# Optimization experiments

Hardware: AMD Instinct MI355X
Metric: run time of the kernel (lower is better)

The kernel has to match this reference:

```python
import jax, jax.numpy as jnp
import numpy as np

B, T, D_MODEL, N_HEADS = 2, 2048, 1024, 16
HEAD_DIM = D_MODEL // N_HEADS
GN_EPS = 1e-5


def decay_gammas(n_heads):
    # gamma_h = 1 - 2^(-5 - h*(8/n_heads))
    h = jnp.arange(n_heads, dtype=jnp.float32)
    return 1.0 - jnp.power(2.0, -5.0 - h * (8.0 / n_heads))


def setup_inputs() -> dict:
    key = jax.random.key(0)
    ks = jax.random.split(key, 7)
    w_scale = 0.02
    return {
        "x": jax.random.normal(ks[0], (B, T, D_MODEL), dtype=jnp.float32),
        "Wq": jax.random.normal(ks[1], (D_MODEL, D_MODEL), dtype=jnp.float32) * w_scale,
        "Wk": jax.random.normal(ks[2], (D_MODEL, D_MODEL), dtype=jnp.float32) * w_scale,
        "Wv": jax.random.normal(ks[3], (D_MODEL, D_MODEL), dtype=jnp.float32) * w_scale,
        "Wo": jax.random.normal(ks[4], (D_MODEL, D_MODEL), dtype=jnp.float32) * w_scale,
        "gn_w": jnp.ones((D_MODEL,), dtype=jnp.float32),
        "gn_b": jnp.zeros((D_MODEL,), dtype=jnp.float32),
    }


def reference(x, Wq, Wk, Wv, Wo, gn_w, gn_b):
    Bx, Tx, C = x.shape
    H, D = N_HEADS, C // N_HEADS
    gammas = decay_gammas(H)  # (H,)

    def split_heads(y):
        return y.reshape(Bx, Tx, H, D).transpose(0, 2, 1, 3)  # (B,H,T,D)

    # torch Linear: y = x @ W.T
    Q = split_heads(x @ Wq.T)
    K = split_heads(x @ Wk.T)
    V = split_heads(x @ Wv.T)

    # causal decay mask D[h,i,j] = gamma_h^(i-j) if i>=j else 0
    idx = jnp.arange(Tx, dtype=jnp.float32)
    diff = idx[:, None] - idx[None, :]  # (T,T)
    mask = jnp.where(diff >= 0,
                     gammas[:, None, None] ** jnp.maximum(diff, 0.0),
                     0.0)  # (H,T,T)

    scores = jnp.einsum("bhtd,bhsd->bhts", Q, K) / jnp.sqrt(jnp.float32(D))
    scores = scores * mask[None]  # (B,H,T,T)
    out = jnp.einsum("bhts,bhsd->bhtd", scores, V)  # (B,H,T,D)
    y = out.transpose(0, 2, 1, 3).reshape(Bx, Tx, C)  # merge heads

    # GroupNorm(n_heads, d_model) applied on (B, C, T): normalizes over
    # (head_dim, T) per group per batch element.
    z = y.transpose(0, 2, 1).reshape(Bx, H, D, Tx)
    mu = z.mean(axis=(2, 3), keepdims=True)
    var = z.var(axis=(2, 3), keepdims=True)
    zn = (z - mu) * jax.lax.rsqrt(var + GN_EPS)
    zn = zn * gn_w.reshape(1, H, D, 1) + gn_b.reshape(1, H, D, 1)
    y = zn.reshape(Bx, C, Tx).transpose(0, 2, 1)  # (B,T,C)

    return y @ Wo.T
```

## Files before the change

kernel.cpp:

```cpp
#include <hip/hip_runtime.h>
#include <hip/hip_bf16.h>

typedef __attribute__((ext_vector_type(8))) short short8;
typedef __attribute__((ext_vector_type(4))) float float4v;
typedef __attribute__((ext_vector_type(16))) float float16v;
typedef unsigned short u16;
typedef unsigned long long ull;

#define KD 1024

__device__ __forceinline__ u16 f2b(float f) {
    __hip_bfloat16 h = __float2bfloat16(f);
    return __builtin_bit_cast(u16, h);
}
__device__ __forceinline__ float b2f(u16 u) {
    unsigned x = ((unsigned)u) << 16;
    return __builtin_bit_cast(float, x);
}
__device__ __forceinline__ float lg_gamma(int h) {
    float gamma = 1.0f - exp2f(-5.0f - 0.5f * (float)h);
    return log2f(gamma);
}

__device__ __forceinline__ void async_cp16(const u16* g, u16* l) {
    __builtin_amdgcn_global_load_lds(
        (const __attribute__((address_space(1))) void*)g,
        (__attribute__((address_space(3))) void*)l,
        16, 0, 0);
}

__global__ __launch_bounds__(256)
void cvt_all(const float* __restrict__ x, const float* __restrict__ wq,
             const float* __restrict__ wk, const float* __restrict__ wv,
             const float* __restrict__ wo,
             u16* __restrict__ xb, u16* __restrict__ wqkvb, u16* __restrict__ wob)
{
    int bid = blockIdx.x;
    const float* src; u16* dst; long off; float sc = 1.0f;
    if (bid < 4096)      { src = x;  dst = xb;              off = (long)bid * 1024; }
    else if (bid < 5120) { src = wq; dst = wqkvb;           off = (long)(bid - 4096) * 1024; sc = 0.125f; }
    else if (bid < 6144) { src = wk; dst = wqkvb + 1048576; off = (long)(bid - 5120) * 1024; }
    else if (bid < 7168) { src = wv; dst = wqkvb + 2097152; off = (long)(bid - 6144) * 1024; }
    else                 { src = wo; dst = wob;             off = (long)(bid - 7168) * 1024; }
    long i = off + threadIdx.x * 4;
    float4 v = *(const float4*)(src + i);
    ushort4 u;
    u.x = f2b(v.x * sc); u.y = f2b(v.y * sc); u.z = f2b(v.z * sc); u.w = f2b(v.w * sc);
    *(ushort4*)(dst + i) = u;
}

template<int MODE>
__global__ __launch_bounds__(256)
void gemm_nt(const u16* __restrict__ A, const u16* __restrict__ Bw,
             u16* __restrict__ oQ, u16* __restrict__ oK,
             u16* __restrict__ oKt, u16* __restrict__ oVt,
             float* __restrict__ of)
{
    constexpr int TM = (MODE == 0) ? 128 : 64;
    constexpr int MI = (MODE == 0) ? 2 : 1;
    __shared__ __attribute__((aligned(16))) u16 Sh[(TM + 128) * 64];
    u16* As = Sh;
    u16* Bs = Sh + TM * 64;
    const int tid = threadIdx.x;
    const int lane = tid & 63;
    const int wv = tid >> 6;
    const int wm = wv >> 1, wn = wv & 1;
    const int row32 = lane & 31, khalf = lane >> 5;
    const int lrow = lane >> 3, lseg = lane & 7;
    const int m0 = blockIdx.y * TM, n0 = blockIdx.x * 128;

    float16v acc[MI][2];
#pragma unroll
    for (int i = 0; i < MI; i++)
#pragma unroll
        for (int j = 0; j < 2; j++)
#pragma unroll
            for (int r = 0; r < 16; r++) acc[i][j][r] = 0.f;

    const int scol = (lseg ^ lrow) << 3;

    for (int kt = 0; kt < KD; kt += 64) {
        __syncthreads();
#pragma unroll
        for (int i = 0; i < TM / 32; i++) {
            int r = wv * (TM / 4) + i * 8;
            async_cp16(A + (size_t)(m0 + r + lrow) * KD + kt + scol, &As[r * 64]);
        }
#pragma unroll
        for (int i = 0; i < 4; i++) {
            int r = wv * 32 + i * 8;
            async_cp16(Bw + (size_t)(n0 + r + lrow) * KD + kt + scol, &Bs[r * 64]);
        }
        __syncthreads();
#pragma unroll
        for (int ks = 0; ks < 4; ks++) {
            short8 af[MI], bf[2];
#pragma unroll
            for (int i = 0; i < MI; i++) {
                int row = wm * (MI * 32) + i * 32 + row32;
                af[i] = *(const short8*)(&As[row * 64 + (((ks * 2 + khalf) ^ (row & 7)) << 3)]);
            }
#pragma unroll
            for (int j = 0; j < 2; j++) {
                int row = wn * 64 + j * 32 + row32;
                bf[j] = *(const short8*)(&Bs[row * 64 + (((ks * 2 + khalf) ^ (row & 7)) << 3)]);
            }
#pragma unroll
            for (int i = 0; i < MI; i++)
#pragma unroll
                for (int j = 0; j < 2; j++)
                    acc[i][j] = __builtin_amdgcn_mfma_f32_32x32x16_bf16(af[i], bf[j], acc[i][j], 0, 0, 0);
        }
    }

    if (MODE == 0) {
        const int wsel = n0 >> 10;
        if (wsel <= 1) {
            u16* dst = (wsel == 0) ? oQ : oK;
#pragma unroll
            for (int i = 0; i < 2; i++)
#pragma unroll
                for (int j = 0; j < 2; j++) {
                    int gn = n0 + wn * 64 + j * 32 + row32;
                    int dd = gn & 63, hh = (gn >> 6) & 15;
#pragma unroll
                    for (int reg = 0; reg < 16; reg++) {
                        int m = m0 + wm * 64 + i * 32 + (reg & 3) + 8 * (reg >> 2) + 4 * khalf;
                        int b = m >> 11, t = m & 2047;
                        dst[(size_t)(b * 16 + hh) * 131072 + t * 64 + dd] = f2b(acc[i][j][reg]);
                    }
                }
        }
        if (wsel >= 1) {
            __syncthreads();
            u16* Tl = Sh + wv * 4096;
#pragma unroll
            for (int i = 0; i < 2; i++)
#pragma unroll
                for (int j = 0; j < 2; j++) {
                    int n_loc = j * 32 + row32;
#pragma unroll
                    for (int g = 0; g < 4; g++) {
                        int m4 = i * 32 + 8 * g + 4 * khalf;
                        ull pk = (ull)f2b(acc[i][j][4 * g]) | ((ull)f2b(acc[i][j][4 * g + 1]) << 16) |
                                 ((ull)f2b(acc[i][j][4 * g + 2]) << 32) | ((ull)f2b(acc[i][j][4 * g + 3]) << 48);
                        *(ull*)(&Tl[n_loc * 64 + (((m4 >> 3) ^ (n_loc & 7)) << 3) + (m4 & 7)]) = pk;
                    }
                }
            __syncthreads();
            int gnb = n0 + wn * 64;
            int hh = (gnb >> 6) & 15;
            int mb = m0 + wm * 64;
            int bh = (mb >> 11) * 16 + hh;
            int t0 = mb & 2047;
            u16* dstT = (wsel == 1) ? oKt : oVt;
            int rr = lane >> 3, ss = lane & 7;
#pragma unroll
            for (int g = 0; g < 8; g++) {
                int row = 8 * g + rr;
                short8 v = *(const short8*)(&Tl[row * 64 + ((ss ^ rr) << 3)]);
                *(short8*)(&dstT[(size_t)bh * 131072 + (size_t)row * 2048 + t0 + ss * 8]) = v;
            }
        }
    } else {
#pragma unroll
        for (int j = 0; j < 2; j++) {
            int gn = n0 + wn * 64 + j * 32 + row32;
#pragma unroll
            for (int reg = 0; reg < 16; reg++) {
                int m = m0 + wm * 32 + (reg & 3) + 8 * (reg >> 2) + 4 * khalf;
                of[(size_t)m * 1024 + gn] = acc[0][j][reg];
            }
        }
    }
}

__global__ __launch_bounds__(256)
void chunk_state(const u16* __restrict__ Kt, const u16* __restrict__ Vt,
                 u16* __restrict__ U)
{
    const int c = blockIdx.x, bh = blockIdx.y, h = bh & 15;
    const int tid = threadIdx.x, lane = tid & 63, w = tid >> 6;
    const int row16 = lane & 15, quad = lane >> 4;
    const float lg = lg_gamma(h);
    const size_t base = (size_t)bh * 131072;

    float4v acc[4];
    float4v zero4 = {0.f, 0.f, 0.f, 0.f};
#pragma unroll
    for (int tn = 0; tn < 4; tn++) acc[tn] = zero4;

#pragma unroll
    for (int kb = 0; kb < 2; kb++) {
        short8 a = *(const short8*)(Vt + base + (size_t)(16 * w + row16) * 2048 + c * 64 + kb * 32 + quad * 8);
        short8 as;
        int e0 = 63 - (kb * 32 + quad * 8);
#pragma unroll
        for (int jj = 0; jj < 8; jj++) {
            float v = b2f((u16)a[jj]) * exp2f(lg * (float)(e0 - jj));
            as[jj] = (short)f2b(v);
        }
#pragma unroll
        for (int tn = 0; tn < 4; tn++) {
            short8 bfr = *(const short8*)(Kt + base + (size_t)(16 * tn + row16) * 2048 + c * 64 + kb * 32 + quad * 8);
            acc[tn] = __builtin_amdgcn_mfma_f32_16x16x32_bf16(as, bfr, acc[tn], 0, 0, 0);
        }
    }
    u16* up = U + ((size_t)bh * 32 + c) * 4096;
#pragma unroll
    for (int tn = 0; tn < 4; tn++)
#pragma unroll
        for (int r = 0; r < 4; r++)
            up[(16 * w + quad * 4 + r) * 64 + 16 * tn + row16] = f2b(acc[tn][r]);
}

__global__ __launch_bounds__(256)
void state_scan(const u16* __restrict__ U, u16* __restrict__ St)
{
    const int bh = blockIdx.y;
    const int e = blockIdx.x * 256 + threadIdx.x;
    const float g64 = exp2f(lg_gamma(bh & 15) * 64.0f);
    float s = 0.f;
    St[(size_t)bh * 131072 + e] = 0;
    for (int c = 1; c < 32; c++) {
        s = g64 * s + b2f(U[((size_t)bh * 32 + (c - 1)) * 4096 + e]);
        St[((size_t)bh * 32 + c) * 4096 + e] = f2b(s);
    }
}

__global__ __launch_bounds__(256)
void retention_chunk(const u16* __restrict__ Q, const u16* __restrict__ Kb,
                     const u16* __restrict__ Vt, const u16* __restrict__ St,
                     float* __restrict__ Y, float* __restrict__ stats)
{
    __shared__ __attribute__((aligned(16))) u16 Pl[4][16 * 72];
    __shared__ float red[8];
    const int c = blockIdx.x, bh = blockIdx.y, h = bh & 15;
    const int tid = threadIdx.x, lane = tid & 63, w = tid >> 6;
    const int row16 = lane & 15, quad = lane >> 4;
    const float lg = lg_gamma(h);
    const size_t base = (size_t)bh * 131072;
    float4v zero4 = {0.f, 0.f, 0.f, 0.f};

    short8 qf[2];
#pragma unroll
    for (int kb = 0; kb < 2; kb++)
        qf[kb] = *(const short8*)(Q + base + (size_t)(c * 64 + 16 * w + row16) * 64 + kb * 32 + quad * 8);

    float4v accp[4];
#pragma unroll
    for (int tn = 0; tn < 4; tn++) accp[tn] = zero4;
#pragma unroll
    for (int tn = 0; tn < 4; tn++)
#pragma unroll
        for (int kb = 0; kb < 2; kb++) {
            short8 kf = *(const short8*)(Kb + base + (size_t)(c * 64 + 16 * tn + row16) * 64 + kb * 32 + quad * 8);
            accp[tn] = __builtin_amdgcn_mfma_f32_16x16x32_bf16(qf[kb], kf, accp[tn], 0, 0, 0);
        }
#pragma unroll
    for (int tn = 0; tn < 4; tn++)
#pragma unroll
        for (int r = 0; r < 4; r++) {
            int a_loc = 16 * w + quad * 4 + r;
            int b_loc = 16 * tn + row16;
            int d = a_loc - b_loc;
            float v = (d >= 0) ? accp[tn][r] * exp2f(lg * (float)d) : 0.f;
            Pl[w][(quad * 4 + r) * 72 + b_loc] = f2b(v);
        }
    __syncthreads();

    short8 pf[2];
#pragma unroll
    for (int kb = 0; kb < 2; kb++)
        pf[kb] = *(const short8*)(&Pl[w][row16 * 72 + kb * 32 + quad * 8]);

    float4v acco[4], acci[4];
#pragma unroll
    for (int tn = 0; tn < 4; tn++) { acco[tn] = zero4; acci[tn] = zero4; }
#pragma unroll
    for (int tn = 0; tn < 4; tn++)
#pragma unroll
        for (int kb = 0; kb < 2; kb++) {
            short8 vf = *(const short8*)(Vt + base + (size_t)(16 * tn + row16) * 2048 + c * 64 + kb * 32 + quad * 8);
            acco[tn] = __builtin_amdgcn_mfma_f32_16x16x32_bf16(pf[kb], vf, acco[tn], 0, 0, 0);
            short8 sf = *(const short8*)(St + ((size_t)bh * 32 + c) * 4096 + (16 * tn + row16) * 64 + kb * 32 + quad * 8);
            acci[tn] = __builtin_amdgcn_mfma_f32_16x16x32_bf16(qf[kb], sf, acci[tn], 0, 0, 0);
        }

    float s = 0.f, s2 = 0.f;
#pragma unroll
    for (int tn = 0; tn < 4; tn++)
#pragma unroll
        for (int r = 0; r < 4; r++) {
            int a_loc = 16 * w + quad * 4 + r;
            float gi = exp2f(lg * (float)(a_loc + 1));
            int t = c * 64 + a_loc, d2 = 16 * tn + row16;
            float yv = acco[tn][r] + gi * acci[tn][r];
            Y[(size_t)bh * 131072 + t * 64 + d2] = yv;
            s += yv;
            s2 += yv * yv;
        }
#pragma unroll
    for (int off = 32; off; off >>= 1) {
        s += __shfl_down(s, off, 64);
        s2 += __shfl_down(s2, off, 64);
    }
    if (lane == 0) { red[w] = s; red[4 + w] = s2; }
    __syncthreads();
    if (tid == 0) {
        atomicAdd(&stats[2 * bh], red[0] + red[1] + red[2] + red[3]);
        atomicAdd(&stats[2 * bh + 1], red[4] + red[5] + red[6] + red[7]);
    }
}

__global__ __launch_bounds__(256)
void gn_apply(const float* __restrict__ Y, const float* __restrict__ stats,
              const float* __restrict__ gnw, const float* __restrict__ gnb,
              u16* __restrict__ Z)
{
    int i4 = (blockIdx.x * 256 + threadIdx.x) * 4;
    int b = i4 >> 21, t = (i4 >> 10) & 2047, cc = i4 & 1023;
    int hh = cc >> 6, dd = cc & 63, bh = b * 16 + hh;
    float4 v = *(const float4*)(Y + (size_t)bh * 131072 + t * 64 + dd);
    float S = stats[2 * bh], S2 = stats[2 * bh + 1];
    float mu = S * (1.0f / 131072.f);
    float var = S2 * (1.0f / 131072.f) - mu * mu;
    float rsg = rsqrtf(var + 1e-5f);
    float4 wv = *(const float4*)(gnw + cc);
    float4 bv = *(const float4*)(gnb + cc);
    ushort4 o;
    o.x = f2b((v.x - mu) * rsg * wv.x + bv.x);
    o.y = f2b((v.y - mu) * rsg * wv.y + bv.y);
    o.z = f2b((v.z - mu) * rsg * wv.z + bv.z);
    o.w = f2b((v.w - mu) * rsg * wv.w + bv.w);
    *(ushort4*)(Z + i4) = o;
}

extern "C" void kernel_launch(void* const* d_in, const int* in_sizes, int n_in,
                              void* d_out, int out_size, void* d_ws, size_t ws_size,
                              hipStream_t stream) {
    const float* x   = (const float*)d_in[0];
    const float* Wq  = (const float*)d_in[1];
    const float* Wk  = (const float*)d_in[2];
    const float* Wv  = (const float*)d_in[3];
    const float* Wo  = (const float*)d_in[4];
    const float* gnw = (const float*)d_in[5];
    const float* gnb = (const float*)d_in[6];
    float* out = (float*)d_out;
    char* ws = (char*)d_ws;

    u16*  xb    = (u16*)(ws + 0);
    u16*  wqkvb = (u16*)(ws + 8388608);
    u16*  wob   = (u16*)(ws + 14680064);
    u16*  Qs    = (u16*)(ws + 16777216);
    u16*  Kb    = (u16*)(ws + 25165824);
    u16*  Kt    = (u16*)(ws + 33554432);
    u16*  Vt    = (u16*)(ws + 41943040);
    u16*  U     = (u16*)(ws + 50331648);
    u16*  St    = (u16*)(ws + 67108864);
    float* Y    = (float*)(ws + 75497472);
    u16*  Zb    = (u16*)(ws + 92274688);
    float* stats= (float*)(ws + 100663296);

    hipMemsetAsync(stats, 0, 64 * sizeof(float), stream);

    cvt_all<<<8192, 256, 0, stream>>>(x, Wq, Wk, Wv, Wo, xb, wqkvb, wob);

    gemm_nt<0><<<dim3(24, 32), 256, 0, stream>>>(xb, wqkvb, Qs, Kb, Kt, Vt, nullptr);

    chunk_state<<<dim3(32, 32), 256, 0, stream>>>(Kt, Vt, U);
    state_scan<<<dim3(16, 32), 256, 0, stream>>>(U, St);
    retention_chunk<<<dim3(32, 32), 256, 0, stream>>>(Qs, Kb, Vt, St, Y, stats);

    gn_apply<<<4096, 256, 0, stream>>>(Y, stats, gnw, gnb, Zb);

    gemm_nt<1><<<dim3(8, 64), 256, 0, stream>>>(Zb, wob, nullptr, nullptr, nullptr, nullptr, out);
}
```

Measured before the change: 188.4 us.

## Load GEMM B operand directly to registers and remap blocks across XCDs

The B (weight) tile is no longer staged through LDS. Each lane instead loads its MFMA B fragments straight from global memory into registers before the barrier. Block indices are remapped so that consecutive M tiles sharing the same N tile land on the same XCD, which is meant to improve L2 reuse of weights. The MODE 1 fp32 output store loop is also reordered. This cuts LDS traffic and barrier-bound staging, but the global loads are uncoalesced per row, raise register pressure, and the load latency is no longer hidden behind an async copy.

```diff
diff --git a/kernel.cpp b/kernel.cpp
--- a/kernel.cpp
+++ b/kernel.cpp
@@ -58,16 +58,20 @@
 {
     constexpr int TM = (MODE == 0) ? 128 : 64;
     constexpr int MI = (MODE == 0) ? 2 : 1;
-    __shared__ __attribute__((aligned(16))) u16 Sh[(TM + 128) * 64];
+    __shared__ __attribute__((aligned(16))) u16 Sh[(MODE == 0) ? 16384 : 4096];
     u16* As = Sh;
-    u16* Bs = Sh + TM * 64;
     const int tid = threadIdx.x;
     const int lane = tid & 63;
     const int wv = tid >> 6;
     const int wm = wv >> 1, wn = wv & 1;
     const int row32 = lane & 31, khalf = lane >> 5;
     const int lrow = lane >> 3, lseg = lane & 7;
-    const int m0 = blockIdx.y * TM, n0 = blockIdx.x * 128;
+    const int lin = blockIdx.x + gridDim.x * blockIdx.y;
+    const int xcd = lin & 7, idx = lin >> 3;
+    int m_tile, n_tile;
+    if (MODE == 0) { m_tile = (idx & 3) + 4 * xcd; n_tile = idx >> 2; }
+    else           { m_tile = (idx & 7) + 8 * xcd; n_tile = idx >> 3; }
+    const int m0 = m_tile * TM, n0 = n_tile * 128;
 
     float16v acc[MI][2];
 #pragma unroll
@@ -78,6 +82,7 @@
             for (int r = 0; r < 16; r++) acc[i][j][r] = 0.f;
 
     const int scol = (lseg ^ lrow) << 3;
+    const u16* bp = Bw + (size_t)(n0 + wn * 64 + row32) * KD + khalf * 8;
 
     for (int kt = 0; kt < KD; kt += 64) {
         __syncthreads();
@@ -86,30 +91,26 @@
             int r = wv * (TM / 4) + i * 8;
             async_cp16(A + (size_t)(m0 + r + lrow) * KD + kt + scol, &As[r * 64]);
         }
-#pragma unroll
-        for (int i = 0; i < 4; i++) {
-            int r = wv * 32 + i * 8;
-            async_cp16(Bw + (size_t)(n0 + r + lrow) * KD + kt + scol, &Bs[r * 64]);
-        }
+        short8 bgl[4][2];
+#pragma unroll
+        for (int ks = 0; ks < 4; ks++)
+#pragma unroll
+            for (int j = 0; j < 2; j++)
+                bgl[ks][j] = *(const short8*)(bp + (size_t)j * 32 * KD + kt + ks * 16);
         __syncthreads();
 #pragma unroll
         for (int ks = 0; ks < 4; ks++) {
-            short8 af[MI], bf[2];
+            short8 af[MI];
 #pragma unroll
             for (int i = 0; i < MI; i++) {
                 int row = wm * (MI * 32) + i * 32 + row32;
                 af[i] = *(const short8*)(&As[row * 64 + (((ks * 2 + khalf) ^ (row & 7)) << 3)]);
             }
 #pragma unroll
-            for (int j = 0; j < 2; j++) {
-                int row = wn * 64 + j * 32 + row32;
-                bf[j] = *(const short8*)(&Bs[row * 64 + (((ks * 2 + khalf) ^ (row & 7)) << 3)]);
-            }
-#pragma unroll
             for (int i = 0; i < MI; i++)
 #pragma unroll
                 for (int j = 0; j < 2; j++)
-                    acc[i][j] = __builtin_amdgcn_mfma_f32_32x32x16_bf16(af[i], bf[j], acc[i][j], 0, 0, 0);
+                    acc[i][j] = __builtin_amdgcn_mfma_f32_32x32x16_bf16(af[i], bgl[ks][j], acc[i][j], 0, 0, 0);
         }
     }
 
@@ -163,15 +164,16 @@
             }
         }
     } else {
-#pragma unroll
-        for (int j = 0; j < 2; j++) {
-            int gn = n0 + wn * 64 + j * 32 + row32;
-#pragma unroll
-            for (int reg = 0; reg < 16; reg++) {
-                int m = m0 + wm * 32 + (reg & 3) + 8 * (reg >> 2) + 4 * khalf;
-                of[(size_t)m * 1024 + gn] = acc[0][j][reg];
+        int gn0 = n0 + wn * 64 + row32;
+#pragma unroll
+        for (int g = 0; g < 4; g++)
+#pragma unroll
+            for (int rr = 0; rr < 4; rr++) {
+                int reg = 4 * g + rr;
+                int m = m0 + wm * 32 + 8 * g + 4 * khalf + rr;
+                of[(size_t)m * 1024 + gn0] = acc[0][0][reg];
+                of[(size_t)m * 1024 + gn0 + 32] = acc[0][1][reg];
             }
-        }
     }
 }
 
```

Result: slower. 227.6 us (+20.8%).
